# Kernel tuning notes

Measured on AMD Instinct MI355X. Metric: run time of the kernel, lower is better.

Reference implementation:

```python
import jax, jax.numpy as jnp
import numpy as np


def setup_inputs() -> dict:
    key = jax.random.key(0)
    k1, k2 = jax.random.split(key)
    flow = jax.random.normal(k1, (4, 2, 256, 256), dtype=jnp.float32)   # [B,2,H,W] per-pixel flow over dt
    spike = jax.random.uniform(k2, (4, 64, 256, 256), dtype=jnp.float32)  # [B,C,H,W] spike voxel grid
    return {"flow": flow, "spike": spike}


def _splat(vals, xn, yn, H, W):
    """Forward bilinear splat of vals [H,W] to continuous coords (xn,yn) [H,W]."""
    x0 = jnp.floor(xn)
    y0 = jnp.floor(yn)
    wx = xn - x0  # fractional weights (differentiable w.r.t. flow)
    wy = yn - y0
    x0i = x0.astype(jnp.int32)
    y0i = y0.astype(jnp.int32)
    out = jnp.zeros(H * W, dtype=vals.dtype)
    corners = (
        (0, 0, (1.0 - wx) * (1.0 - wy)),
        (1, 0, wx * (1.0 - wy)),
        (0, 1, (1.0 - wx) * wy),
        (1, 1, wx * wy),
    )
    for dx, dy, w in corners:
        xi = x0i + dx
        yi = y0i + dy
        valid = (xi >= 0) & (xi < W) & (yi >= 0) & (yi < H)
        idx = jnp.clip(yi, 0, H - 1) * W + jnp.clip(xi, 0, W - 1)
        out = out.at[idx.ravel()].add(jnp.where(valid, w * vals, 0.0).ravel())
    return out.reshape(H, W)


def spike_warp_mid(spike, flow, dt):
    """Warp each time bin c by flow * (c - mid)/dt toward the middle timestamp (bilinear splat)."""
    B, C, H, W = spike.shape
    mid = (C - 1) / 2.0
    yy, xx = jnp.meshgrid(jnp.arange(H, dtype=spike.dtype),
                          jnp.arange(W, dtype=spike.dtype), indexing='ij')
    s = (jnp.arange(C, dtype=spike.dtype) - mid) / jnp.asarray(dt, spike.dtype)  # [C]
    u = flow[:, 0][:, None]  # [B,1,H,W]
    v = flow[:, 1][:, None]
    xn = xx + u * s[None, :, None, None]  # [B,C,H,W]
    yn = yy + v * s[None, :, None, None]
    splat_bc = jax.vmap(jax.vmap(lambda va, xa, ya: _splat(va, xa, ya, H, W)))
    return splat_bc(spike, xn, yn)  # [B,C,H,W]


def reference(flow, spike):
    B, C, H, W = spike.shape
    spike_warped = spike_warp_mid(spike, flow, dt=64)
    # Faithful to original: sum over BATCH dim inside per-batch loop (same each iter),
    # so loss = (B * -var) / B = -var(spike_image) with unbiased variance.
    spike_image = jnp.sum(spike_warped, axis=0)  # [C,H,W]
    loss = -jnp.var(spike_image - jnp.mean(spike_image), ddof=1)
    return loss
```

## Files before the change

kernel.cpp:

```cpp
#include <hip/hip_runtime.h>

typedef float f2 __attribute__((ext_vector_type(2)));
typedef float f4v __attribute__((ext_vector_type(4)));

constexpr int B = 4, C = 64, H = 256, W = 256;
constexpr int HW = H * W;
constexpr long long N_TOT = (long long)C * HW;

constexpr int TS = 16;
constexpr int INW = 18;
constexpr int INA = INW * INW;
constexpr int OVW = 19;
constexpr int OVH = 18;
constexpr int OVA = OVH * OVW;
constexpr int NBLK = 256 * 8;

__global__ __launch_bounds__(256) void fused_kernel(
    const float* __restrict__ flow,
    const float* __restrict__ spike,
    double* __restrict__ partials) {
  __shared__ __align__(16) f4v spkA[INA];
  __shared__ __align__(16) f4v spkB[INA];
  __shared__ f2 uv[INA];
  __shared__ __align__(16) float ovf[8 * OVA];
  __shared__ double red[8];

  const int bid = blockIdx.x;
  const int tile = bid & 255;
  const int j = bid >> 8;
  const int tx0 = (tile & 15) * TS;
  const int ty0 = (tile >> 4) * TS;
  const int tid = threadIdx.x;
  const int qx = tid & 15, qy = tid >> 4;
  const int wave = tid >> 6;

  {
    f4v z = {0.f, 0.f, 0.f, 0.f};
    f4v* ov4 = (f4v*)ovf;
    for (int i = tid; i < (8 * OVA) / 4; i += 256) ov4[i] = z;
  }

  f2 smv[4];
  float sm[4];
#pragma unroll
  for (int t = 0; t < 4; ++t) {
    float s = ((float)(4 * j + t) + 0.5f) * (1.0f / 64.0f);
    sm[t] = s;
    smv[t] = f2{-s, s};
  }
  const int cn0 = 31 - 4 * j;
  const int cp0 = 32 + 4 * j;
  const int Rj = (j >> 1) + 1;
  const int SWj = TS + 2 * Rj;
  const int SAj = SWj * SWj;

  bool c_act[3], c_val[3], c_inn[3];
  int c_gp[3], c_ip[3];
  float c_px[3], c_py[3];
#pragma unroll
  for (int k = 0; k < 3; ++k) {
    int pos = tid + 256 * k;
    bool act = pos < SAj;
    int row = act ? pos / SWj : 0;
    int col = pos - row * SWj;
    int relx = col - Rj, rely = row - Rj;
    int gy = ty0 + rely, gx = tx0 + relx;
    c_act[k] = act;
    c_val[k] = act & ((unsigned)gy < (unsigned)H) & ((unsigned)gx < (unsigned)W);
    c_gp[k] = gy * W + gx;
    c_inn[k] = act & (relx >= -1) & (relx <= 16) & (rely >= -1) & (rely <= 16);
    c_ip[k] = (rely + 1) * INW + (relx + 1);
    c_px[k] = (float)relx;
    c_py[k] = (float)rely;
  }

  float p_u[3], p_v[3];
  float4 p_a[3], p_b[3];

  auto prefetch = [&](int bb) {
    const float* fu = flow + (size_t)bb * 2 * HW;
    const float* fv = fu + HW;
    const float* spb = spike + (size_t)bb * C * HW;
#pragma unroll
    for (int k = 0; k < 3; ++k) {
      float u = 0.f, v = 0.f;
      float4 a = {0.f, 0.f, 0.f, 0.f};
      float4 d = {0.f, 0.f, 0.f, 0.f};
      if (c_val[k]) {
        int gp = c_gp[k];
        u = fu[gp];
        v = fv[gp];
        a.x = spb[(size_t)cn0 * HW + gp];
        a.y = spb[(size_t)(cn0 - 1) * HW + gp];
        a.z = spb[(size_t)(cn0 - 2) * HW + gp];
        a.w = spb[(size_t)(cn0 - 3) * HW + gp];
        d.x = spb[(size_t)cp0 * HW + gp];
        d.y = spb[(size_t)(cp0 + 1) * HW + gp];
        d.z = spb[(size_t)(cp0 + 2) * HW + gp];
        d.w = spb[(size_t)(cp0 + 3) * HW + gp];
      }
      p_u[k] = u; p_v[k] = v; p_a[k] = a; p_b[k] = d;
    }
  };

  prefetch(0);
  __syncthreads();

  const int qip = (qy + 1) * INW + (qx + 1);
  f2 acc2[4];
#pragma unroll
  for (int t = 0; t < 4; ++t) acc2[t] = f2{0.f, 0.f};

  for (int bb = 0; bb < B; ++bb) {
#pragma unroll
    for (int k = 0; k < 3; ++k) {
      if (!c_act[k]) continue;
      float u = p_u[k], v = p_v[k];
      float4 a = p_a[k], d = p_b[k];
      float es = fmaxf(fabsf(u), fabsf(v));
      bool ev0 = es * sm[0] >= 1.0f;
      bool ev1 = es * sm[1] >= 1.0f;
      bool ev2 = es * sm[2] >= 1.0f;
      bool ev3 = es * sm[3] >= 1.0f;
      if (c_inn[k]) {
        int ip = c_ip[k];
        uv[ip] = f2{u, v};
        spkA[ip] = f4v{ev0 ? 0.f : a.x, ev0 ? 0.f : d.x,
                       ev1 ? 0.f : a.y, ev1 ? 0.f : d.y};
        spkB[ip] = f4v{ev2 ? 0.f : a.z, ev2 ? 0.f : d.z,
                       ev3 ? 0.f : a.w, ev3 ? 0.f : d.w};
      }
      if (__any(ev3)) {
        const f2 u2 = f2{u, u}, v2 = f2{v, v};
        const f2 px2 = f2{c_px[k], c_px[k]}, py2 = f2{c_py[k], c_py[k]};
        const float av[4] = {a.x, a.y, a.z, a.w};
        const float bv[4] = {d.x, d.y, d.z, d.w};
#pragma unroll
        for (int t = 0; t < 4; ++t) {
          bool ev = es * sm[t] >= 1.0f;
          if (ev) {
            f2 xn = __builtin_elementwise_fma(u2, smv[t], px2);
            f2 yn = __builtin_elementwise_fma(v2, smv[t], py2);
#pragma unroll
            for (int h = 0; h < 2; ++h) {
              float x = xn[h], y = yn[h];
              float val = h ? bv[t] : av[t];
              float fx = floorf(x), fy = floorf(y);
              float f = x - fx, g = y - fy;
              int X0 = (int)fx, Y0 = (int)fy;
              int ix0 = ((unsigned)X0 < 16u) ? X0 + 1 : 17;
              int ix1 = ((unsigned)(X0 + 1) < 16u) ? X0 + 2 : 18;
              int iy0 = ((unsigned)Y0 < 16u) ? Y0 + 1 : 17;
              int iy1 = ((unsigned)(Y0 + 1) < 16u) ? Y0 + 2 : 17;
              float* pl = &ovf[(2 * t + h) * OVA];
              float w1 = f * val, w0 = val - w1;
              float g1 = g, g0 = 1.0f - g;
              atomicAdd(pl + iy0 * OVW + ix0, w0 * g0);
              atomicAdd(pl + iy0 * OVW + ix1, w1 * g0);
              atomicAdd(pl + iy1 * OVW + ix0, w0 * g1);
              atomicAdd(pl + iy1 * OVW + ix1, w1 * g1);
            }
          }
        }
      }
    }
    __syncthreads();
    if (bb + 1 < B) prefetch(bb + 1);

#pragma unroll
    for (int dy = -1; dy <= 1; ++dy) {
#pragma unroll
      for (int dx = -1; dx <= 1; ++dx) {
        const int ip = qip + dy * INW + dx;
        const f2 u2v = uv[ip];
        const f4v A = spkA[ip];
        const f4v Bv = spkB[ip];
        const f2 ux = f2{u2v.x, u2v.x};
        const f2 vy = f2{u2v.y, u2v.y};
        const f2 fdx2 = (float)dx;
        const f2 fdy2 = (float)dy;
        const f2 vals[4] = {f2{A[0], A[1]}, f2{A[2], A[3]},
                            f2{Bv[0], Bv[1]}, f2{Bv[2], Bv[3]}};
#pragma unroll
        for (int t = 0; t < 4; ++t) {
          f2 ax = __builtin_elementwise_fma(ux, smv[t], fdx2);
          f2 ay = __builtin_elementwise_fma(vy, smv[t], fdy2);
          f2 tx, ty;
          tx[0] = __builtin_amdgcn_fmed3f(1.0f - fabsf(ax[0]), 0.f, 1.f);
          tx[1] = __builtin_amdgcn_fmed3f(1.0f - fabsf(ax[1]), 0.f, 1.f);
          ty[0] = __builtin_amdgcn_fmed3f(1.0f - fabsf(ay[0]), 0.f, 1.f);
          ty[1] = __builtin_amdgcn_fmed3f(1.0f - fabsf(ay[1]), 0.f, 1.f);
          acc2[t] = __builtin_elementwise_fma(tx * ty, vals[t], acc2[t]);
        }
      }
    }
    __syncthreads();
  }

  const int oip = (qy + 1) * OVW + (qx + 1);
#pragma unroll
  for (int t = 0; t < 4; ++t) {
    acc2[t] += f2{ovf[(2 * t) * OVA + oip], ovf[(2 * t + 1) * OVA + oip]};
  }

  double ls = 0.0, lq = 0.0;
#pragma unroll
  for (int t = 0; t < 4; ++t) {
    double a = (double)acc2[t].x, b2 = (double)acc2[t].y;
    ls += a + b2;
    lq += a * a + b2 * b2;
  }
  for (int off = 32; off > 0; off >>= 1) {
    ls += __shfl_down(ls, off, 64);
    lq += __shfl_down(lq, off, 64);
  }
  if ((tid & 63) == 0) { red[wave * 2] = ls; red[wave * 2 + 1] = lq; }
  __syncthreads();
  if (tid == 0) {
    partials[2 * bid] = red[0] + red[2] + red[4] + red[6];
    partials[2 * bid + 1] = red[1] + red[3] + red[5] + red[7];
  }
}

__global__ __launch_bounds__(256) void finalize_kernel(
    const double* __restrict__ partials, float* __restrict__ out) {
  double s = 0.0, q = 0.0;
  for (int i = threadIdx.x; i < NBLK; i += 256) {
    s += partials[2 * i];
    q += partials[2 * i + 1];
  }
  for (int off = 32; off > 0; off >>= 1) {
    s += __shfl_down(s, off, 64);
    q += __shfl_down(q, off, 64);
  }
  __shared__ double ss[4], qq[4];
  int lane = threadIdx.x & 63;
  int wave = threadIdx.x >> 6;
  if (lane == 0) { ss[wave] = s; qq[wave] = q; }
  __syncthreads();
  if (threadIdx.x == 0) {
    double sum = ss[0] + ss[1] + ss[2] + ss[3];
    double sq = qq[0] + qq[1] + qq[2] + qq[3];
    double n = (double)N_TOT;
    double var = (sq - sum * sum / n) / (n - 1.0);
    out[0] = (float)(-var);
  }
}

extern "C" void kernel_launch(void* const* d_in, const int* in_sizes, int n_in,
                              void* d_out, int out_size, void* d_ws, size_t ws_size,
                              hipStream_t stream) {
  const float* flow = (const float*)d_in[0];
  const float* spike = (const float*)d_in[1];
  float* out = (float*)d_out;
  double* partials = (double*)d_ws;

  fused_kernel<<<dim3(NBLK), dim3(256), 0, stream>>>(flow, spike, partials);
  finalize_kernel<<<1, dim3(256), 0, stream>>>(partials, out);
}
```

Baseline: 148.6 us.

## Split tiles to 16x8 and divide channel group across two half-blocks

Shrinks the spatial tile to 16x8 and has each 128-thread half of a block handle two of the four channel pairs, doubling the block count and halving per-thread register state. Adds a launch-bounds occupancy hint and swizzles the block-to-channel-group mapping to balance the heavier high-displacement groups across the grid. The smaller tile raises the halo-to-interior ratio, so more redundant global loads and more overflow atomics fall outside the tile.

```diff
diff --git a/kernel.cpp b/kernel.cpp
--- a/kernel.cpp
+++ b/kernel.cpp
@@ -7,31 +7,34 @@
 constexpr int HW = H * W;
 constexpr long long N_TOT = (long long)C * HW;
 
-constexpr int TS = 16;
-constexpr int INW = 18;
-constexpr int INA = INW * INW;
-constexpr int OVW = 19;
-constexpr int OVH = 18;
-constexpr int OVA = OVH * OVW;
-constexpr int NBLK = 256 * 8;
-
-__global__ __launch_bounds__(256) void fused_kernel(
+constexpr int TW = 16, TH = 8;
+constexpr int INW = 18, INH = 10;
+constexpr int INA = INW * INH;
+constexpr int OVW = 19, OVH = 10;
+constexpr int OVA = OVW * OVH;
+constexpr int NPART = 512;
+constexpr int NBLK = NPART * 8;
+
+__global__ __launch_bounds__(256, 6) void fused_kernel(
     const float* __restrict__ flow,
     const float* __restrict__ spike,
     double* __restrict__ partials) {
-  __shared__ __align__(16) f4v spkA[INA];
-  __shared__ __align__(16) f4v spkB[INA];
+  __shared__ __align__(16) f4v spk0[INA];
+  __shared__ __align__(16) f4v spk1[INA];
   __shared__ f2 uv[INA];
   __shared__ __align__(16) float ovf[8 * OVA];
   __shared__ double red[8];
 
   const int bid = blockIdx.x;
-  const int tile = bid & 255;
-  const int j = bid >> 8;
-  const int tx0 = (tile & 15) * TS;
-  const int ty0 = (tile >> 4) * TS;
+  const int part = bid >> 3;
+  const int j = 7 - ((bid ^ (bid >> 3)) & 7);
+  const int tx0 = (part & 15) * TW;
+  const int ty0 = (part >> 4) * TH;
   const int tid = threadIdx.x;
-  const int qx = tid & 15, qy = tid >> 4;
+  const int l = tid & 127;
+  const int half = tid >> 7;
+  const int tb = 2 * half;
+  const int qx = l & 15, qy = l >> 4;
   const int wave = tid >> 6;
 
   {
@@ -40,26 +43,26 @@
     for (int i = tid; i < (8 * OVA) / 4; i += 256) ov4[i] = z;
   }
 
-  f2 smv[4];
-  float sm[4];
-#pragma unroll
-  for (int t = 0; t < 4; ++t) {
-    float s = ((float)(4 * j + t) + 0.5f) * (1.0f / 64.0f);
-    sm[t] = s;
-    smv[t] = f2{-s, s};
-  }
-  const int cn0 = 31 - 4 * j;
-  const int cp0 = 32 + 4 * j;
+  f2 smv[2];
+  float sm[2];
+#pragma unroll
+  for (int tt = 0; tt < 2; ++tt) {
+    float s = ((float)(4 * j + tb + tt) + 0.5f) * (1.0f / 64.0f);
+    sm[tt] = s;
+    smv[tt] = f2{-s, s};
+  }
+  const int cn = 31 - 4 * j - tb;
+  const int cp = 32 + 4 * j + tb;
   const int Rj = (j >> 1) + 1;
-  const int SWj = TS + 2 * Rj;
-  const int SAj = SWj * SWj;
+  const int SWj = TW + 2 * Rj;
+  const int SAj = SWj * (TH + 2 * Rj);
 
   bool c_act[3], c_val[3], c_inn[3];
   int c_gp[3], c_ip[3];
   float c_px[3], c_py[3];
 #pragma unroll
   for (int k = 0; k < 3; ++k) {
-    int pos = tid + 256 * k;
+    int pos = l + 128 * k;
     bool act = pos < SAj;
     int row = act ? pos / SWj : 0;
     int col = pos - row * SWj;
@@ -68,14 +71,14 @@
     c_act[k] = act;
     c_val[k] = act & ((unsigned)gy < (unsigned)H) & ((unsigned)gx < (unsigned)W);
     c_gp[k] = gy * W + gx;
-    c_inn[k] = act & (relx >= -1) & (relx <= 16) & (rely >= -1) & (rely <= 16);
+    c_inn[k] = act & (relx >= -1) & (relx <= TW) & (rely >= -1) & (rely <= TH);
     c_ip[k] = (rely + 1) * INW + (relx + 1);
     c_px[k] = (float)relx;
     c_py[k] = (float)rely;
   }
 
   float p_u[3], p_v[3];
-  float4 p_a[3], p_b[3];
+  float4 p_s[3];
 
   auto prefetch = [&](int bb) {
     const float* fu = flow + (size_t)bb * 2 * HW;
@@ -84,22 +87,17 @@
 #pragma unroll
     for (int k = 0; k < 3; ++k) {
       float u = 0.f, v = 0.f;
-      float4 a = {0.f, 0.f, 0.f, 0.f};
-      float4 d = {0.f, 0.f, 0.f, 0.f};
+      float4 s4 = {0.f, 0.f, 0.f, 0.f};
       if (c_val[k]) {
         int gp = c_gp[k];
         u = fu[gp];
         v = fv[gp];
-        a.x = spb[(size_t)cn0 * HW + gp];
-        a.y = spb[(size_t)(cn0 - 1) * HW + gp];
-        a.z = spb[(size_t)(cn0 - 2) * HW + gp];
-        a.w = spb[(size_t)(cn0 - 3) * HW + gp];
-        d.x = spb[(size_t)cp0 * HW + gp];
-        d.y = spb[(size_t)(cp0 + 1) * HW + gp];
-        d.z = spb[(size_t)(cp0 + 2) * HW + gp];
-        d.w = spb[(size_t)(cp0 + 3) * HW + gp];
-      }
-      p_u[k] = u; p_v[k] = v; p_a[k] = a; p_b[k] = d;
+        s4.x = spb[(size_t)cn * HW + gp];
+        s4.y = spb[(size_t)cp * HW + gp];
+        s4.z = spb[(size_t)(cn - 1) * HW + gp];
+        s4.w = spb[(size_t)(cp + 1) * HW + gp];
+      }
+      p_u[k] = u; p_v[k] = v; p_s[k] = s4;
     }
   };
 
@@ -107,52 +105,50 @@
   __syncthreads();
 
   const int qip = (qy + 1) * INW + (qx + 1);
-  f2 acc2[4];
-#pragma unroll
-  for (int t = 0; t < 4; ++t) acc2[t] = f2{0.f, 0.f};
+  const f4v* spkH = half ? spk1 : spk0;
+  f2 acc2[2];
+  acc2[0] = f2{0.f, 0.f};
+  acc2[1] = f2{0.f, 0.f};
 
   for (int bb = 0; bb < B; ++bb) {
 #pragma unroll
     for (int k = 0; k < 3; ++k) {
       if (!c_act[k]) continue;
       float u = p_u[k], v = p_v[k];
-      float4 a = p_a[k], d = p_b[k];
+      float4 s4 = p_s[k];
       float es = fmaxf(fabsf(u), fabsf(v));
       bool ev0 = es * sm[0] >= 1.0f;
       bool ev1 = es * sm[1] >= 1.0f;
-      bool ev2 = es * sm[2] >= 1.0f;
-      bool ev3 = es * sm[3] >= 1.0f;
       if (c_inn[k]) {
         int ip = c_ip[k];
-        uv[ip] = f2{u, v};
-        spkA[ip] = f4v{ev0 ? 0.f : a.x, ev0 ? 0.f : d.x,
-                       ev1 ? 0.f : a.y, ev1 ? 0.f : d.y};
-        spkB[ip] = f4v{ev2 ? 0.f : a.z, ev2 ? 0.f : d.z,
-                       ev3 ? 0.f : a.w, ev3 ? 0.f : d.w};
-      }
-      if (__any(ev3)) {
+        if (half == 0) uv[ip] = f2{u, v};
+        f4v* dst = half ? spk1 : spk0;
+        dst[ip] = f4v{ev0 ? 0.f : s4.x, ev0 ? 0.f : s4.y,
+                      ev1 ? 0.f : s4.z, ev1 ? 0.f : s4.w};
+      }
+      if (__any(ev1)) {
         const f2 u2 = f2{u, u}, v2 = f2{v, v};
         const f2 px2 = f2{c_px[k], c_px[k]}, py2 = f2{c_py[k], c_py[k]};
-        const float av[4] = {a.x, a.y, a.z, a.w};
-        const float bv[4] = {d.x, d.y, d.z, d.w};
-#pragma unroll
-        for (int t = 0; t < 4; ++t) {
-          bool ev = es * sm[t] >= 1.0f;
+        const float nv[2] = {s4.x, s4.z};
+        const float pv[2] = {s4.y, s4.w};
+#pragma unroll
+        for (int tt = 0; tt < 2; ++tt) {
+          bool ev = es * sm[tt] >= 1.0f;
           if (ev) {
-            f2 xn = __builtin_elementwise_fma(u2, smv[t], px2);
-            f2 yn = __builtin_elementwise_fma(v2, smv[t], py2);
+            f2 xn = __builtin_elementwise_fma(u2, smv[tt], px2);
+            f2 yn = __builtin_elementwise_fma(v2, smv[tt], py2);
 #pragma unroll
             for (int h = 0; h < 2; ++h) {
               float x = xn[h], y = yn[h];
-              float val = h ? bv[t] : av[t];
+              float val = h ? pv[tt] : nv[tt];
               float fx = floorf(x), fy = floorf(y);
               float f = x - fx, g = y - fy;
               int X0 = (int)fx, Y0 = (int)fy;
-              int ix0 = ((unsigned)X0 < 16u) ? X0 + 1 : 17;
-              int ix1 = ((unsigned)(X0 + 1) < 16u) ? X0 + 2 : 18;
-              int iy0 = ((unsigned)Y0 < 16u) ? Y0 + 1 : 17;
-              int iy1 = ((unsigned)(Y0 + 1) < 16u) ? Y0 + 2 : 17;
-              float* pl = &ovf[(2 * t + h) * OVA];
+              int ix0 = ((unsigned)X0 < (unsigned)TW) ? X0 + 1 : 17;
+              int ix1 = ((unsigned)(X0 + 1) < (unsigned)TW) ? X0 + 2 : 18;
+              int iy0 = ((unsigned)Y0 < (unsigned)TH) ? Y0 + 1 : 9;
+              int iy1 = ((unsigned)(Y0 + 1) < (unsigned)TH) ? Y0 + 2 : 9;
+              float* pl = &ovf[(2 * (tb + tt) + h) * OVA];
               float w1 = f * val, w0 = val - w1;
               float g1 = g, g0 = 1.0f - g;
               atomicAdd(pl + iy0 * OVW + ix0, w0 * g0);
@@ -173,24 +169,22 @@
       for (int dx = -1; dx <= 1; ++dx) {
         const int ip = qip + dy * INW + dx;
         const f2 u2v = uv[ip];
-        const f4v A = spkA[ip];
-        const f4v Bv = spkB[ip];
+        const f4v A = spkH[ip];
         const f2 ux = f2{u2v.x, u2v.x};
         const f2 vy = f2{u2v.y, u2v.y};
         const f2 fdx2 = (float)dx;
         const f2 fdy2 = (float)dy;
-        const f2 vals[4] = {f2{A[0], A[1]}, f2{A[2], A[3]},
-                            f2{Bv[0], Bv[1]}, f2{Bv[2], Bv[3]}};
-#pragma unroll
-        for (int t = 0; t < 4; ++t) {
-          f2 ax = __builtin_elementwise_fma(ux, smv[t], fdx2);
-          f2 ay = __builtin_elementwise_fma(vy, smv[t], fdy2);
+        const f2 vals[2] = {f2{A[0], A[1]}, f2{A[2], A[3]}};
+#pragma unroll
+        for (int tt = 0; tt < 2; ++tt) {
+          f2 ax = __builtin_elementwise_fma(ux, smv[tt], fdx2);
+          f2 ay = __builtin_elementwise_fma(vy, smv[tt], fdy2);
           f2 tx, ty;
           tx[0] = __builtin_amdgcn_fmed3f(1.0f - fabsf(ax[0]), 0.f, 1.f);
           tx[1] = __builtin_amdgcn_fmed3f(1.0f - fabsf(ax[1]), 0.f, 1.f);
           ty[0] = __builtin_amdgcn_fmed3f(1.0f - fabsf(ay[0]), 0.f, 1.f);
           ty[1] = __builtin_amdgcn_fmed3f(1.0f - fabsf(ay[1]), 0.f, 1.f);
-          acc2[t] = __builtin_elementwise_fma(tx * ty, vals[t], acc2[t]);
+          acc2[tt] = __builtin_elementwise_fma(tx * ty, vals[tt], acc2[tt]);
         }
       }
     }
@@ -199,14 +193,15 @@
 
   const int oip = (qy + 1) * OVW + (qx + 1);
 #pragma unroll
-  for (int t = 0; t < 4; ++t) {
-    acc2[t] += f2{ovf[(2 * t) * OVA + oip], ovf[(2 * t + 1) * OVA + oip]};
+  for (int tt = 0; tt < 2; ++tt) {
+    acc2[tt] += f2{ovf[(2 * (tb + tt)) * OVA + oip],
+                   ovf[(2 * (tb + tt) + 1) * OVA + oip]};
   }
 
   double ls = 0.0, lq = 0.0;
 #pragma unroll
-  for (int t = 0; t < 4; ++t) {
-    double a = (double)acc2[t].x, b2 = (double)acc2[t].y;
+  for (int tt = 0; tt < 2; ++tt) {
+    double a = (double)acc2[tt].x, b2 = (double)acc2[tt].y;
     ls += a + b2;
     lq += a * a + b2 * b2;
   }
```

Measured after the change: 208.3 us. 40.2% more time.

## Skip unneeded spike loads, reorder block mapping, and simplify gather weights

Applied to the files above, without the earlier changes.

Spike loads for halo pixels are now issued only when the pixel lies in the inner gather region or needs the large-displacement atomic splat path. Flow loads come first to decide this, and the software prefetch of the next batch is removed. Block-to-tile mapping changes so the eight time-bin groups of one tile are adjacent, with j swizzled for load balance. Gather weights are specialised per neighbour offset, the overflow buffer is shrunk, and one sync is dropped. The cost is that load latency is no longer hidden behind the previous batch's compute.

```diff
diff --git a/kernel.cpp b/kernel.cpp
--- a/kernel.cpp
+++ b/kernel.cpp
@@ -8,28 +8,27 @@
 constexpr long long N_TOT = (long long)C * HW;
 
 constexpr int TS = 16;
-constexpr int INW = 18;
-constexpr int INA = INW * INW;
-constexpr int OVW = 19;
-constexpr int OVH = 18;
-constexpr int OVA = OVH * OVW;
-constexpr int NBLK = 256 * 8;
+constexpr int PPS = 19;
+constexpr int PPA = PPS * 18;
+constexpr int OVW = 17;
+constexpr int OVA = OVW * OVW;
+constexpr int NBLK = 2048;
 
 __global__ __launch_bounds__(256) void fused_kernel(
     const float* __restrict__ flow,
     const float* __restrict__ spike,
     double* __restrict__ partials) {
-  __shared__ __align__(16) f4v spkA[INA];
-  __shared__ __align__(16) f4v spkB[INA];
-  __shared__ f2 uv[INA];
+  __shared__ __align__(16) f4v pl01[PPA];
+  __shared__ __align__(16) f4v pl23[PPA];
+  __shared__ f2 uvp[PPA];
   __shared__ __align__(16) float ovf[8 * OVA];
   __shared__ double red[8];
 
   const int bid = blockIdx.x;
-  const int tile = bid & 255;
-  const int j = bid >> 8;
-  const int tx0 = (tile & 15) * TS;
-  const int ty0 = (tile >> 4) * TS;
+  const int part = bid >> 3;
+  const int j = 7 - ((bid ^ (bid >> 3)) & 7);
+  const int tx0 = (part & 15) * TS;
+  const int ty0 = (part >> 4) * TS;
   const int tid = threadIdx.x;
   const int qx = tid & 15, qy = tid >> 4;
   const int wave = tid >> 6;
@@ -41,11 +40,9 @@
   }
 
   f2 smv[4];
-  float sm[4];
 #pragma unroll
   for (int t = 0; t < 4; ++t) {
     float s = ((float)(4 * j + t) + 0.5f) * (1.0f / 64.0f);
-    sm[t] = s;
     smv[t] = f2{-s, s};
   }
   const int cn0 = 31 - 4 * j;
@@ -53,10 +50,10 @@
   const int Rj = (j >> 1) + 1;
   const int SWj = TS + 2 * Rj;
   const int SAj = SWj * SWj;
-
-  bool c_act[3], c_val[3], c_inn[3];
-  int c_gp[3], c_ip[3];
-  float c_px[3], c_py[3];
+  const int sbg = (ty0 - Rj) * W + (tx0 - Rj);
+
+  int c_rc[3];
+  int c_meta[3];
 #pragma unroll
   for (int k = 0; k < 3; ++k) {
     int pos = tid + 256 * k;
@@ -65,94 +62,84 @@
     int col = pos - row * SWj;
     int relx = col - Rj, rely = row - Rj;
     int gy = ty0 + rely, gx = tx0 + relx;
-    c_act[k] = act;
-    c_val[k] = act & ((unsigned)gy < (unsigned)H) & ((unsigned)gx < (unsigned)W);
-    c_gp[k] = gy * W + gx;
-    c_inn[k] = act & (relx >= -1) & (relx <= 16) & (rely >= -1) & (rely <= 16);
-    c_ip[k] = (rely + 1) * INW + (relx + 1);
-    c_px[k] = (float)relx;
-    c_py[k] = (float)rely;
-  }
-
-  float p_u[3], p_v[3];
-  float4 p_a[3], p_b[3];
-
-  auto prefetch = [&](int bb) {
+    bool val = act & ((unsigned)gy < (unsigned)H) & ((unsigned)gx < (unsigned)W);
+    bool inn = act & (relx >= -1) & (relx <= 16) & (rely >= -1) & (rely <= 16);
+    c_rc[k] = (row << 8) | col;
+    c_meta[k] = (int)act | ((int)val << 1) | ((int)inn << 2);
+  }
+
+  __syncthreads();
+
+  const int qb = (qy + 1) * PPS + (qx + 1);
+  f2 acc2[4];
+#pragma unroll
+  for (int t = 0; t < 4; ++t) acc2[t] = f2{0.f, 0.f};
+
+  for (int bb = 0; bb < B; ++bb) {
     const float* fu = flow + (size_t)bb * 2 * HW;
     const float* fv = fu + HW;
     const float* spb = spike + (size_t)bb * C * HW;
+
 #pragma unroll
     for (int k = 0; k < 3; ++k) {
+      const int meta = c_meta[k];
+      if (!(meta & 1)) continue;
+      const int row = c_rc[k] >> 8, col = c_rc[k] & 255;
+      const int gp = sbg + c_rc[k];
+      const bool valb = (meta & 2) != 0;
+      const bool innb = (meta & 4) != 0;
       float u = 0.f, v = 0.f;
-      float4 a = {0.f, 0.f, 0.f, 0.f};
-      float4 d = {0.f, 0.f, 0.f, 0.f};
-      if (c_val[k]) {
-        int gp = c_gp[k];
-        u = fu[gp];
-        v = fv[gp];
-        a.x = spb[(size_t)cn0 * HW + gp];
-        a.y = spb[(size_t)(cn0 - 1) * HW + gp];
-        a.z = spb[(size_t)(cn0 - 2) * HW + gp];
-        a.w = spb[(size_t)(cn0 - 3) * HW + gp];
-        d.x = spb[(size_t)cp0 * HW + gp];
-        d.y = spb[(size_t)(cp0 + 1) * HW + gp];
-        d.z = spb[(size_t)(cp0 + 2) * HW + gp];
-        d.w = spb[(size_t)(cp0 + 3) * HW + gp];
-      }
-      p_u[k] = u; p_v[k] = v; p_a[k] = a; p_b[k] = d;
-    }
-  };
-
-  prefetch(0);
-  __syncthreads();
-
-  const int qip = (qy + 1) * INW + (qx + 1);
-  f2 acc2[4];
-#pragma unroll
-  for (int t = 0; t < 4; ++t) acc2[t] = f2{0.f, 0.f};
-
-  for (int bb = 0; bb < B; ++bb) {
-#pragma unroll
-    for (int k = 0; k < 3; ++k) {
-      if (!c_act[k]) continue;
-      float u = p_u[k], v = p_v[k];
-      float4 a = p_a[k], d = p_b[k];
-      float es = fmaxf(fabsf(u), fabsf(v));
-      bool ev0 = es * sm[0] >= 1.0f;
-      bool ev1 = es * sm[1] >= 1.0f;
-      bool ev2 = es * sm[2] >= 1.0f;
-      bool ev3 = es * sm[3] >= 1.0f;
-      if (c_inn[k]) {
-        int ip = c_ip[k];
-        uv[ip] = f2{u, v};
-        spkA[ip] = f4v{ev0 ? 0.f : a.x, ev0 ? 0.f : d.x,
-                       ev1 ? 0.f : a.y, ev1 ? 0.f : d.y};
-        spkB[ip] = f4v{ev2 ? 0.f : a.z, ev2 ? 0.f : d.z,
-                       ev3 ? 0.f : a.w, ev3 ? 0.f : d.w};
+      if (valb) { u = fu[gp]; v = fv[gp]; }
+      const float es = fmaxf(fabsf(u), fabsf(v));
+      const bool ev0 = es * smv[0].y >= 1.0f;
+      const bool ev1 = es * smv[1].y >= 1.0f;
+      const bool ev2 = es * smv[2].y >= 1.0f;
+      const bool ev3 = es * smv[3].y >= 1.0f;
+      float n0 = 0.f, n1 = 0.f, n2 = 0.f, n3 = 0.f;
+      float p0 = 0.f, p1 = 0.f, p2 = 0.f, p3 = 0.f;
+      if (valb && (innb || ev3)) {
+        n0 = spb[(size_t)cn0 * HW + gp];
+        n1 = spb[(size_t)(cn0 - 1) * HW + gp];
+        n2 = spb[(size_t)(cn0 - 2) * HW + gp];
+        n3 = spb[(size_t)(cn0 - 3) * HW + gp];
+        p0 = spb[(size_t)cp0 * HW + gp];
+        p1 = spb[(size_t)(cp0 + 1) * HW + gp];
+        p2 = spb[(size_t)(cp0 + 2) * HW + gp];
+        p3 = spb[(size_t)(cp0 + 3) * HW + gp];
+      }
+      if (innb) {
+        const int relx = col - Rj, rely = row - Rj;
+        const int ips = (rely + 1) * PPS + (relx + 1);
+        uvp[ips] = f2{u, v};
+        pl01[ips] = f4v{ev0 ? 0.f : n0, ev0 ? 0.f : p0,
+                        ev1 ? 0.f : n1, ev1 ? 0.f : p1};
+        pl23[ips] = f4v{ev2 ? 0.f : n2, ev2 ? 0.f : p2,
+                        ev3 ? 0.f : n3, ev3 ? 0.f : p3};
       }
       if (__any(ev3)) {
+        const float px = (float)(col - Rj), py = (float)(row - Rj);
         const f2 u2 = f2{u, u}, v2 = f2{v, v};
-        const f2 px2 = f2{c_px[k], c_px[k]}, py2 = f2{c_py[k], c_py[k]};
-        const float av[4] = {a.x, a.y, a.z, a.w};
-        const float bv[4] = {d.x, d.y, d.z, d.w};
-#pragma unroll
-        for (int t = 0; t < 4; ++t) {
-          bool ev = es * sm[t] >= 1.0f;
+        const f2 px2 = f2{px, px}, py2 = f2{py, py};
+        const float nv[4] = {n0, n1, n2, n3};
+        const float pv[4] = {p0, p1, p2, p3};
+#pragma unroll
+        for (int tt = 0; tt < 4; ++tt) {
+          const bool ev = es * smv[tt].y >= 1.0f;
           if (ev) {
-            f2 xn = __builtin_elementwise_fma(u2, smv[t], px2);
-            f2 yn = __builtin_elementwise_fma(v2, smv[t], py2);
+            f2 xn = __builtin_elementwise_fma(u2, smv[tt], px2);
+            f2 yn = __builtin_elementwise_fma(v2, smv[tt], py2);
 #pragma unroll
             for (int h = 0; h < 2; ++h) {
               float x = xn[h], y = yn[h];
-              float val = h ? bv[t] : av[t];
+              float val = h ? pv[tt] : nv[tt];
               float fx = floorf(x), fy = floorf(y);
               float f = x - fx, g = y - fy;
               int X0 = (int)fx, Y0 = (int)fy;
-              int ix0 = ((unsigned)X0 < 16u) ? X0 + 1 : 17;
-              int ix1 = ((unsigned)(X0 + 1) < 16u) ? X0 + 2 : 18;
-              int iy0 = ((unsigned)Y0 < 16u) ? Y0 + 1 : 17;
-              int iy1 = ((unsigned)(Y0 + 1) < 16u) ? Y0 + 2 : 17;
-              float* pl = &ovf[(2 * t + h) * OVA];
+              int ix0 = ((unsigned)X0 < 16u) ? X0 : 16;
+              int ix1 = ((unsigned)(X0 + 1) < 16u) ? X0 + 1 : 16;
+              int iy0 = ((unsigned)Y0 < 16u) ? Y0 : 16;
+              int iy1 = ((unsigned)(Y0 + 1) < 16u) ? Y0 + 1 : 16;
+              float* pl = &ovf[(2 * tt + h) * OVA];
               float w1 = f * val, w0 = val - w1;
               float g1 = g, g0 = 1.0f - g;
               atomicAdd(pl + iy0 * OVW + ix0, w0 * g0);
@@ -165,48 +152,47 @@
       }
     }
     __syncthreads();
-    if (bb + 1 < B) prefetch(bb + 1);
 
 #pragma unroll
     for (int dy = -1; dy <= 1; ++dy) {
 #pragma unroll
       for (int dx = -1; dx <= 1; ++dx) {
-        const int ip = qip + dy * INW + dx;
-        const f2 u2v = uv[ip];
-        const f4v A = spkA[ip];
-        const f4v Bv = spkB[ip];
-        const f2 ux = f2{u2v.x, u2v.x};
-        const f2 vy = f2{u2v.y, u2v.y};
-        const f2 fdx2 = (float)dx;
-        const f2 fdy2 = (float)dy;
+        const int ip = qb + dy * PPS + dx;
+        const f2 uvv = uvp[ip];
+        const f4v A = pl01[ip];
+        const f4v Bv = pl23[ip];
+        const f2 u2 = f2{uvv.x, uvv.x};
+        const f2 v2 = f2{uvv.y, uvv.y};
         const f2 vals[4] = {f2{A[0], A[1]}, f2{A[2], A[3]},
                             f2{Bv[0], Bv[1]}, f2{Bv[2], Bv[3]}};
 #pragma unroll
-        for (int t = 0; t < 4; ++t) {
-          f2 ax = __builtin_elementwise_fma(ux, smv[t], fdx2);
-          f2 ay = __builtin_elementwise_fma(vy, smv[t], fdy2);
-          f2 tx, ty;
-          tx[0] = __builtin_amdgcn_fmed3f(1.0f - fabsf(ax[0]), 0.f, 1.f);
-          tx[1] = __builtin_amdgcn_fmed3f(1.0f - fabsf(ax[1]), 0.f, 1.f);
-          ty[0] = __builtin_amdgcn_fmed3f(1.0f - fabsf(ay[0]), 0.f, 1.f);
-          ty[1] = __builtin_amdgcn_fmed3f(1.0f - fabsf(ay[1]), 0.f, 1.f);
-          acc2[t] = __builtin_elementwise_fma(tx * ty, vals[t], acc2[t]);
+        for (int tt = 0; tt < 4; ++tt) {
+          const f2 dxv = u2 * smv[tt];
+          const f2 dyv = v2 * smv[tt];
+          f2 wx, wy;
+          if (dx < 0)      wx = __builtin_elementwise_max(dxv, f2{0.f, 0.f});
+          else if (dx > 0) wx = __builtin_elementwise_max(f2{0.f, 0.f} - dxv, f2{0.f, 0.f});
+          else { wx.x = 1.0f - fabsf(dxv.x); wx.y = 1.0f - fabsf(dxv.y); }
+          if (dy < 0)      wy = __builtin_elementwise_max(dyv, f2{0.f, 0.f});
+          else if (dy > 0) wy = __builtin_elementwise_max(f2{0.f, 0.f} - dyv, f2{0.f, 0.f});
+          else { wy.x = 1.0f - fabsf(dyv.x); wy.y = 1.0f - fabsf(dyv.y); }
+          acc2[tt] = __builtin_elementwise_fma(wx * wy, vals[tt], acc2[tt]);
         }
       }
     }
-    __syncthreads();
-  }
-
-  const int oip = (qy + 1) * OVW + (qx + 1);
-#pragma unroll
-  for (int t = 0; t < 4; ++t) {
-    acc2[t] += f2{ovf[(2 * t) * OVA + oip], ovf[(2 * t + 1) * OVA + oip]};
+    if (bb + 1 < B) __syncthreads();
+  }
+
+  const int oip = qy * OVW + qx;
+#pragma unroll
+  for (int tt = 0; tt < 4; ++tt) {
+    acc2[tt] += f2{ovf[(2 * tt) * OVA + oip], ovf[(2 * tt + 1) * OVA + oip]};
   }
 
   double ls = 0.0, lq = 0.0;
 #pragma unroll
-  for (int t = 0; t < 4; ++t) {
-    double a = (double)acc2[t].x, b2 = (double)acc2[t].y;
+  for (int tt = 0; tt < 4; ++tt) {
+    double a = (double)acc2[tt].x, b2 = (double)acc2[tt].y;
     ls += a + b2;
     lq += a * a + b2 * b2;
   }
```

After: 169.9 us. 1.14x slower.
